# Kernel optimization log

Hardware: AMD Instinct MI355X
Metric: run time of the kernel (lower is better)

The kernel has to match this reference:

```python
import jax, jax.numpy as jnp
import numpy as np

B, T, NF, D, H = 4, 32, 256, 512, 8
DK = D // H


def setup_inputs() -> dict:
    key = jax.random.key(0)
    ks = jax.random.split(key, 10)
    x = jax.random.normal(ks[0], (B, T, NF, D), dtype=jnp.float32)
    adj = jax.random.randint(ks[1], (NF, NF), 0, 2, dtype=jnp.int32)
    adj = adj.at[jnp.arange(NF), jnp.arange(NF)].set(1)  # self-loops avoid all-masked rows
    s = 1.0 / np.sqrt(D)
    Wq = jax.random.normal(ks[2], (D, D), dtype=jnp.float32) * s
    Wk = jax.random.normal(ks[3], (D, D), dtype=jnp.float32) * s
    Wv = jax.random.normal(ks[4], (D, D), dtype=jnp.float32) * s
    Wo = jax.random.normal(ks[5], (D, D), dtype=jnp.float32) * s
    bq = jnp.zeros((D,), jnp.float32)
    bk = jnp.zeros((D,), jnp.float32)
    bv = jnp.zeros((D,), jnp.float32)
    bo = jnp.zeros((D,), jnp.float32)
    return {"x": x, "adj": adj, "Wq": Wq, "bq": bq, "Wk": Wk, "bk": bk,
            "Wv": Wv, "bv": bv, "Wo": Wo, "bo": bo}


def reference(x, adj, Wq, bq, Wk, bk, Wv, bv, Wo, bo):
    b, t, nf, d = x.shape
    q = x @ Wq.T + bq
    k = x @ Wk.T + bk
    v = x @ Wv.T + bv
    # split heads: [B,T,Nf,H,dk]
    qh = q.reshape(b, t, nf, H, DK)
    kh = k.reshape(b, t, nf, H, DK)
    vh = v.reshape(b, t, nf, H, DK)
    scores = jnp.einsum('btihd,btjhd->bthij', qh, kh) / jnp.sqrt(jnp.float32(DK))
    mask = (adj > 0)  # [Nf,Nf], broadcast over b,t,h
    scores = jnp.where(mask[None, None, None], scores, jnp.float32(-jnp.inf))
    attn = jax.nn.softmax(scores, axis=-1)  # dropout is identity in eval
    out = jnp.einsum('bthij,btjhd->btihd', attn, vh).reshape(b, t, nf, d)
    return out @ Wo.T + bo
```

## Files before the change

### kernel.cpp

```cpp
#include <hip/hip_runtime.h>

#define NF 256
#define H_ 8
#define M_ 32768

typedef _Float16 f16;
typedef _Float16 f16x8 __attribute__((ext_vector_type(8)));
typedef float f32x4 __attribute__((ext_vector_type(4)));
typedef unsigned short u16x8 __attribute__((ext_vector_type(8)));

#define GLOAD16(src, dst) \
  __builtin_amdgcn_global_load_lds((const __attribute__((address_space(1))) void*)(src), \
                                   (__attribute__((address_space(3))) void*)(dst), 16, 0, 0)

#define LDS_FENCE() do { asm volatile("s_waitcnt lgkmcnt(0)" ::: "memory"); \
                         __builtin_amdgcn_sched_barrier(0); } while (0)

template <int NR>
__device__ __forceinline__ void stage_rows(const f16* __restrict__ g, int ld, int row0, int coff,
                                           f16* ldsb, int wave, int lane) {
    const int rr = wave * 8 + (lane >> 3);
    const int p  = lane & 7;
#pragma unroll
    for (int i = 0; i < NR / 32; ++i) {
        int r = i * 32 + rr;
        int col = ((p ^ (r & 7)) << 3);
        GLOAD16(g + (size_t)(row0 + r) * ld + coff + col, ldsb + (i * 32 + wave * 8) * 64);
    }
}

template <int NR>
__device__ __forceinline__ void stage_rows512(const f16* __restrict__ g, int ld, int coff,
                                              f16* ldsb, int wave, int lane) {
    const int rr = wave * 8 + (lane >> 3);
    const int p  = lane & 7;
#pragma unroll
    for (int i = 0; i < NR / 64; ++i) {
        int r = i * 64 + rr;
        int col = ((p ^ (r & 7)) << 3);
        GLOAD16(g + (size_t)r * ld + coff + col, ldsb + (i * 64 + wave * 8) * 64);
    }
}


__global__ void cvt_x(const float* __restrict__ src, f16* __restrict__ dst, int n8) {
    int idx = blockIdx.x * blockDim.x + threadIdx.x;
    int stride = gridDim.x * blockDim.x;
    for (; idx < n8; idx += stride) {
        const float4* s = reinterpret_cast<const float4*>(src + (size_t)idx * 8);
        float4 v0 = s[0], v1 = s[1];
        f16x8 o;
        o[0] = (f16)v0.x; o[1] = (f16)v0.y; o[2] = (f16)v0.z; o[3] = (f16)v0.w;
        o[4] = (f16)v1.x; o[5] = (f16)v1.y; o[6] = (f16)v1.z; o[7] = (f16)v1.w;
        *reinterpret_cast<f16x8*>(dst + (size_t)idx * 8) = o;
    }
}

#define QSCALE 0.1803368801111204f

__global__ void prep(const float* __restrict__ Wq, const float* __restrict__ Wk,
                     const float* __restrict__ Wv, const float* __restrict__ Wo,
                     const float* __restrict__ bq, const float* __restrict__ bk,
                     const float* __restrict__ bv, const int* __restrict__ adj,
                     f16* __restrict__ Wh, f16* __restrict__ Woh,
                     float* __restrict__ biasAll, unsigned long long* __restrict__ bmask) {
    const int tid = blockIdx.x * 256 + threadIdx.x;
    {
        const float* s; f16* d; float sc = 1.0f;
        int pp = tid >> 15, off = tid & 32767;
        if (pp == 0)      { s = Wq; d = Wh;              sc = QSCALE; }
        else if (pp == 1) { s = Wk; d = Wh + 512 * 512; }
        else if (pp == 2) { s = Wv; d = Wh + 2 * 512 * 512; }
        else              { s = Wo; d = Woh; }
        const float4* sv4 = reinterpret_cast<const float4*>(s + (size_t)off * 8);
        float4 v0 = sv4[0], v1 = sv4[1];
        f16x8 o;
        o[0] = (f16)(v0.x * sc); o[1] = (f16)(v0.y * sc);
        o[2] = (f16)(v0.z * sc); o[3] = (f16)(v0.w * sc);
        o[4] = (f16)(v1.x * sc); o[5] = (f16)(v1.y * sc);
        o[6] = (f16)(v1.z * sc); o[7] = (f16)(v1.w * sc);
        *reinterpret_cast<f16x8*>(d + (size_t)off * 8) = o;
    }
    if (tid < 1536) {
        float v = (tid < 512) ? QSCALE * bq[tid] : (tid < 1024) ? bk[tid - 512] : bv[tid - 1024];
        biasAll[tid] = v;
    }
    if (tid < 65536) {
        unsigned long long bal = __ballot(adj[tid] > 0);
        if ((tid & 63) == 0) bmask[tid >> 6] = bal;
    }
}


__global__ __launch_bounds__(256) void qkv_gemm(const f16* __restrict__ A, const f16* __restrict__ W,
                                                const float* __restrict__ biasAll,
                                                f16* __restrict__ out) {
    __shared__ f16 lds[32768];
    const int t = threadIdx.x, wave = t >> 6, lane = t & 63;
    const int l15 = lane & 15, l4 = lane >> 4;
    const int m0 = blockIdx.x * 128, n0 = blockIdx.y * 128;
    const int wr = wave >> 1, wc = wave & 1;
    f32x4 acc[4][4] = {};

    stage_rows<128>(A, 512, m0, 0, lds, wave, lane);
    stage_rows<128>(W, 512, n0, 0, lds + 8192, wave, lane);
    __syncthreads();
    int cur = 0;
    for (int kt = 0; kt < 8; ++kt) {
        if (kt < 7) {
            stage_rows<128>(A, 512, m0, (kt + 1) * 64, lds + (cur ^ 1) * 16384, wave, lane);
            stage_rows<128>(W, 512, n0, (kt + 1) * 64, lds + (cur ^ 1) * 16384 + 8192, wave, lane);
        }
        const f16* Ab = lds + cur * 16384;
        const f16* Bb = Ab + 8192;
        f16x8 af[4][2], bf[4][2];
#pragma unroll
        for (int i = 0; i < 4; ++i)
#pragma unroll
            for (int kk = 0; kk < 2; ++kk) {
                int ra = wr * 64 + i * 16 + l15;
                int rb = wc * 64 + i * 16 + l15;
                int s = kk * 4 + l4;
                af[i][kk] = *reinterpret_cast<const f16x8*>(Ab + ra * 64 + ((s ^ (ra & 7)) << 3));
                bf[i][kk] = *reinterpret_cast<const f16x8*>(Bb + rb * 64 + ((s ^ (rb & 7)) << 3));
            }
#pragma unroll
        for (int i = 0; i < 4; ++i)
#pragma unroll
            for (int j = 0; j < 4; ++j)
#pragma unroll
                for (int kk = 0; kk < 2; ++kk)
                    acc[i][j] = __builtin_amdgcn_mfma_f32_16x16x32_f16(af[i][kk], bf[j][kk], acc[i][j], 0, 0, 0);
        __syncthreads();
        cur ^= 1;
    }
    {
        f16* Es = lds;
#pragma unroll
        for (int i = 0; i < 4; ++i)
#pragma unroll
            for (int j = 0; j < 4; ++j) {
                int lc = wc * 64 + j * 16 + l15;
                float bb = biasAll[n0 + lc];
#pragma unroll
                for (int r = 0; r < 4; ++r) {
                    int lr = wr * 64 + i * 16 + l4 * 4 + r;
                    Es[lr * 132 + lc] = (f16)(acc[i][j][r] + bb);
                }
            }
        __syncthreads();
        const int rrow = t >> 4, slot = t & 15;
#pragma unroll
        for (int p2 = 0; p2 < 8; ++p2) {
            int r = p2 * 16 + rrow;
            *reinterpret_cast<f16x8*>(out + (size_t)(m0 + r) * 1536 + n0 + slot * 8) =
                *reinterpret_cast<const f16x8*>(Es + r * 132 + slot * 8);
        }
    }
}


__global__ __launch_bounds__(512) void attn_kernel(const f16* __restrict__ qkv,
                                                   const unsigned long long* __restrict__ bmg,
                                                   f16* __restrict__ ao) {
    __shared__ f16 Ks[256 * 64];
    __shared__ f16 Vs[64 * 256];
    __shared__ f16 Ps[8][16][264];
    __shared__ unsigned long long BMs[1024];
    const int t = threadIdx.x, wave = t >> 6, lane = t & 63;
    const int l15 = lane & 15, l4 = lane >> 4;
    const int bh = blockIdx.x, bt = bh >> 3, h = bh & 7;
    const int btq = bt * 256, hq = h * 64;
    const f16* qb = qkv + (size_t)btq * 1536 + hq;
    const f16* kb = qkv + (size_t)btq * 1536 + 512 + hq;
    const f16* vb = qkv + (size_t)btq * 1536 + 1024 + hq;

    stage_rows512<256>(kb, 1536, 0, Ks, wave, lane);
    GLOAD16((const char*)bmg + (size_t)t * 16, (char*)(BMs + wave * 128));
    {
        const int slot = t & 7, r0 = t >> 3;
#pragma unroll
        for (int i = 0; i < 4; ++i) {
            int nf = r0 + i * 64;
            f16x8 v = *reinterpret_cast<const f16x8*>(vb + (size_t)nf * 1536 + slot * 8);
#pragma unroll
            for (int e = 0; e < 8; ++e) {
                int dk = slot * 8 + e;
                int key = (dk & 7) ^ (dk >> 3);
                Vs[dk * 256 + (((nf >> 3) ^ key) << 3) + (nf & 7)] = v[e];
            }
        }
    }
    __syncthreads();

    for (int s = 0; s < 2; ++s) {
        const int qrow_base = wave * 32 + s * 16;

        f16x8 aq[2];
#pragma unroll
        for (int kk = 0; kk < 2; ++kk)
            aq[kk] = *reinterpret_cast<const f16x8*>(
                qb + (size_t)(qrow_base + l15) * 1536 + kk * 32 + l4 * 8);

        f32x4 sacc[16];
#pragma unroll
        for (int ct = 0; ct < 16; ++ct) sacc[ct] = (f32x4){0.f, 0.f, 0.f, 0.f};
#pragma unroll
        for (int ct = 0; ct < 16; ++ct)
#pragma unroll
            for (int kk = 0; kk < 2; ++kk) {
                int rk = ct * 16 + l15;
                int sk = kk * 4 + l4;
                f16x8 bk_ = *reinterpret_cast<const f16x8*>(Ks + rk * 64 + ((sk ^ (rk & 7)) << 3));
                sacc[ct] = __builtin_amdgcn_mfma_f32_16x16x32_f16(aq[kk], bk_, sacc[ct], 0, 0, 0);
            }

        LDS_FENCE();

        float rs[4];
#pragma unroll
        for (int r = 0; r < 4; ++r) {
            const int ig = qrow_base + l4 * 4 + r;
            const u16x8* mr = reinterpret_cast<const u16x8*>(BMs + ig * 4);
            u16x8 w0 = mr[0], w1 = mr[1];
            float mx = -1e38f;
#pragma unroll
            for (int ct = 0; ct < 16; ++ct) mx = fmaxf(mx, sacc[ct][r]);
#pragma unroll
            for (int m = 1; m < 16; m <<= 1) mx = fmaxf(mx, __shfl_xor(mx, m, 64));
            float sum = 0.f;
#pragma unroll
            for (int ct = 0; ct < 16; ++ct) {
                unsigned wbit = (ct < 8) ? (unsigned)w0[ct] : (unsigned)w1[ct & 7];
                float p = __builtin_exp2f(sacc[ct][r] - mx);
                p = ((wbit >> l15) & 1u) ? p : 0.0f;
                sacc[ct][r] = p;
                sum += p;
            }
#pragma unroll
            for (int m = 1; m < 16; m <<= 1) sum += __shfl_xor(sum, m, 64);
            rs[r] = 1.0f / sum;
#pragma unroll
            for (int ct = 0; ct < 16; ++ct)
                Ps[wave][l4 * 4 + r][ct * 16 + l15] = (f16)sacc[ct][r];
        }

        LDS_FENCE();

        f32x4 oacc[4] = {};
#pragma unroll
        for (int kk = 0; kk < 8; ++kk) {
            f16x8 ap = *reinterpret_cast<const f16x8*>(&Ps[wave][l15][kk * 32 + l4 * 8]);
#pragma unroll
            for (int c2 = 0; c2 < 4; ++c2) {
                int dk = c2 * 16 + l15;
                int key = (dk & 7) ^ (dk >> 3);
                int sv = kk * 4 + l4;
                f16x8 bv_ = *reinterpret_cast<const f16x8*>(Vs + dk * 256 + ((sv ^ key) << 3));
                oacc[c2] = __builtin_amdgcn_mfma_f32_16x16x32_f16(ap, bv_, oacc[c2], 0, 0, 0);
            }
        }
#pragma unroll
        for (int c2 = 0; c2 < 4; ++c2)
#pragma unroll
            for (int r = 0; r < 4; ++r) {
                int nf = qrow_base + l4 * 4 + r;
                int dcol = hq + c2 * 16 + l15;
                ao[((size_t)btq + nf) * 512 + dcol] = (f16)(oacc[c2][r] * rs[r]);
            }
    }
}


__global__ __launch_bounds__(256) void o_gemm(const f16* __restrict__ A, const f16* __restrict__ W,
                                              const float* __restrict__ bo, float* __restrict__ out) {
    __shared__ f16 lds[32768];
    const int t = threadIdx.x, wave = t >> 6, lane = t & 63;
    const int l15 = lane & 15, l4 = lane >> 4;
    const int m0 = blockIdx.x * 128, n0 = blockIdx.y * 128;
    const int wr = wave >> 1, wc = wave & 1;
    f32x4 acc[4][4] = {};

    stage_rows<128>(A, 512, m0, 0, lds, wave, lane);
    stage_rows<128>(W, 512, n0, 0, lds + 8192, wave, lane);
    __syncthreads();
    int cur = 0;
    for (int kt = 0; kt < 8; ++kt) {
        if (kt < 7) {
            stage_rows<128>(A, 512, m0, (kt + 1) * 64, lds + (cur ^ 1) * 16384, wave, lane);
            stage_rows<128>(W, 512, n0, (kt + 1) * 64, lds + (cur ^ 1) * 16384 + 8192, wave, lane);
        }
        const f16* Ab = lds + cur * 16384;
        const f16* Bb = Ab + 8192;
        f16x8 af[4][2], bf[4][2];
#pragma unroll
        for (int i = 0; i < 4; ++i)
#pragma unroll
            for (int kk = 0; kk < 2; ++kk) {
                int ra = wr * 64 + i * 16 + l15;
                int rb = wc * 64 + i * 16 + l15;
                int s = kk * 4 + l4;
                af[i][kk] = *reinterpret_cast<const f16x8*>(Ab + ra * 64 + ((s ^ (ra & 7)) << 3));
                bf[i][kk] = *reinterpret_cast<const f16x8*>(Bb + rb * 64 + ((s ^ (rb & 7)) << 3));
            }
#pragma unroll
        for (int i = 0; i < 4; ++i)
#pragma unroll
            for (int j = 0; j < 4; ++j)
#pragma unroll
                for (int kk = 0; kk < 2; ++kk)
                    acc[i][j] = __builtin_amdgcn_mfma_f32_16x16x32_f16(af[i][kk], bf[j][kk], acc[i][j], 0, 0, 0);
        __syncthreads();
        cur ^= 1;
    }
#pragma unroll
    for (int i = 0; i < 4; ++i)
#pragma unroll
        for (int j = 0; j < 4; ++j) {
            int ng = n0 + wc * 64 + j * 16 + l15;
            float bb = bo[ng];
#pragma unroll
            for (int r = 0; r < 4; ++r) {
                int mg = m0 + wr * 64 + i * 16 + l4 * 4 + r;
                out[(size_t)mg * 512 + ng] = acc[i][j][r] + bb;
            }
        }
}


extern "C" void kernel_launch(void* const* d_in, const int* in_sizes, int n_in,
                              void* d_out, int out_size, void* d_ws, size_t ws_size,
                              hipStream_t stream) {
    const float* x   = (const float*)d_in[0];
    const int*   adj = (const int*)d_in[1];
    const float* Wq  = (const float*)d_in[2];
    const float* bq  = (const float*)d_in[3];
    const float* Wk  = (const float*)d_in[4];
    const float* bk  = (const float*)d_in[5];
    const float* Wv  = (const float*)d_in[6];
    const float* bv  = (const float*)d_in[7];
    const float* Wo  = (const float*)d_in[8];
    const float* bo  = (const float*)d_in[9];
    float* out = (float*)d_out;

    char* ws = (char*)d_ws;
    f16*   Wh      = (f16*)ws;
    f16*   Woh     = (f16*)(ws + 1572864);
    float* biasAll = (float*)(ws + 2097152);
    unsigned long long* bmask = (unsigned long long*)(ws + 2103296);
    f16*   xh      = (f16*)(ws + 2111488);
    f16*   qkvb    = (f16*)(ws + 2111488 + (size_t)M_ * 512 * 2);
    f16*   aob     = xh;

    cvt_x<<<2048, 256, 0, stream>>>(x, xh, M_ * 512 / 8);
    prep<<<512, 256, 0, stream>>>(Wq, Wk, Wv, Wo, bq, bk, bv, adj, Wh, Woh, biasAll, bmask);
    qkv_gemm<<<dim3(M_ / 128, 12), 256, 0, stream>>>(xh, Wh, biasAll, qkvb);
    attn_kernel<<<128 * H_, 512, 0, stream>>>(qkvb, bmask, aob);
    o_gemm<<<dim3(M_ / 128, 4), 256, 0, stream>>>(aob, Woh, bo, out);
}
```

Measured before the change: 204.1 us.

## Halve GEMM K-tile to shrink LDS and remap blocks for XCD locality

Both GEMMs move from a K-tile of 64 to 32, which halves the double-buffered LDS footprint (64KB to 32KB, with a union for the qkv epilogue) and uses a new 4-chunk swizzle. This is meant to let more blocks be resident per CU. The grid becomes 1D with an XCD-aware mapping so blocks sharing A rows land on the same XCD and reuse L2. The cost is twice as many K iterations and barriers, with fewer MFMAs between each sync.

```diff
diff --git a/kernel.cpp b/kernel.cpp
--- a/kernel.cpp
+++ b/kernel.cpp
@@ -17,15 +17,15 @@
                          __builtin_amdgcn_sched_barrier(0); } while (0)
 
 template <int NR>
-__device__ __forceinline__ void stage_rows(const f16* __restrict__ g, int ld, int row0, int coff,
-                                           f16* ldsb, int wave, int lane) {
-    const int rr = wave * 8 + (lane >> 3);
-    const int p  = lane & 7;
-#pragma unroll
-    for (int i = 0; i < NR / 32; ++i) {
-        int r = i * 32 + rr;
-        int col = ((p ^ (r & 7)) << 3);
-        GLOAD16(g + (size_t)(row0 + r) * ld + coff + col, ldsb + (i * 32 + wave * 8) * 64);
+__device__ __forceinline__ void stage32(const f16* __restrict__ g, int ld, int row0, int coff,
+                                        f16* ldsb, int wave, int lane) {
+    const int rr = wave * 16 + (lane >> 2);
+    const int p  = lane & 3;
+#pragma unroll
+    for (int i = 0; i < NR / 64; ++i) {
+        int r = i * 64 + rr;
+        int col = ((p ^ ((r >> 1) & 3)) << 3);
+        GLOAD16(g + (size_t)(row0 + r) * ld + coff + col, ldsb + (i * 64 + wave * 16) * 32);
     }
 }
 
@@ -95,47 +95,48 @@
 __global__ __launch_bounds__(256) void qkv_gemm(const f16* __restrict__ A, const f16* __restrict__ W,
                                                 const float* __restrict__ biasAll,
                                                 f16* __restrict__ out) {
-    __shared__ f16 lds[32768];
+    __shared__ union { f16 stage[16384]; f16 epi[128 * 132]; } u;
     const int t = threadIdx.x, wave = t >> 6, lane = t & 63;
     const int l15 = lane & 15, l4 = lane >> 4;
-    const int m0 = blockIdx.x * 128, n0 = blockIdx.y * 128;
+    const int lb = blockIdx.x;
+    const int xcd = lb & 7, idx = lb >> 3;
+    const int m0 = (xcd * 32 + idx / 12) * 128;
+    const int n0 = (idx % 12) * 128;
     const int wr = wave >> 1, wc = wave & 1;
     f32x4 acc[4][4] = {};
 
-    stage_rows<128>(A, 512, m0, 0, lds, wave, lane);
-    stage_rows<128>(W, 512, n0, 0, lds + 8192, wave, lane);
+    stage32<128>(A, 512, m0, 0, u.stage, wave, lane);
+    stage32<128>(W, 512, n0, 0, u.stage + 4096, wave, lane);
     __syncthreads();
     int cur = 0;
-    for (int kt = 0; kt < 8; ++kt) {
-        if (kt < 7) {
-            stage_rows<128>(A, 512, m0, (kt + 1) * 64, lds + (cur ^ 1) * 16384, wave, lane);
-            stage_rows<128>(W, 512, n0, (kt + 1) * 64, lds + (cur ^ 1) * 16384 + 8192, wave, lane);
-        }
-        const f16* Ab = lds + cur * 16384;
-        const f16* Bb = Ab + 8192;
-        f16x8 af[4][2], bf[4][2];
+    for (int kt = 0; kt < 16; ++kt) {
+        if (kt < 15) {
+            stage32<128>(A, 512, m0, (kt + 1) * 32, u.stage + (cur ^ 1) * 8192, wave, lane);
+            stage32<128>(W, 512, n0, (kt + 1) * 32, u.stage + (cur ^ 1) * 8192 + 4096, wave, lane);
+        }
+        const f16* Ab = u.stage + cur * 8192;
+        const f16* Bb = Ab + 4096;
+        f16x8 af[4], bf[4];
+#pragma unroll
+        for (int i = 0; i < 4; ++i) {
+            int ra = wr * 64 + i * 16 + l15;
+            af[i] = *reinterpret_cast<const f16x8*>(Ab + ra * 32 + ((l4 ^ ((ra >> 1) & 3)) << 3));
+        }
+#pragma unroll
+        for (int j = 0; j < 4; ++j) {
+            int rb = wc * 64 + j * 16 + l15;
+            bf[j] = *reinterpret_cast<const f16x8*>(Bb + rb * 32 + ((l4 ^ ((rb >> 1) & 3)) << 3));
+        }
 #pragma unroll
         for (int i = 0; i < 4; ++i)
 #pragma unroll
-            for (int kk = 0; kk < 2; ++kk) {
-                int ra = wr * 64 + i * 16 + l15;
-                int rb = wc * 64 + i * 16 + l15;
-                int s = kk * 4 + l4;
-                af[i][kk] = *reinterpret_cast<const f16x8*>(Ab + ra * 64 + ((s ^ (ra & 7)) << 3));
-                bf[i][kk] = *reinterpret_cast<const f16x8*>(Bb + rb * 64 + ((s ^ (rb & 7)) << 3));
-            }
-#pragma unroll
-        for (int i = 0; i < 4; ++i)
-#pragma unroll
             for (int j = 0; j < 4; ++j)
-#pragma unroll
-                for (int kk = 0; kk < 2; ++kk)
-                    acc[i][j] = __builtin_amdgcn_mfma_f32_16x16x32_f16(af[i][kk], bf[j][kk], acc[i][j], 0, 0, 0);
+                acc[i][j] = __builtin_amdgcn_mfma_f32_16x16x32_f16(af[i], bf[j], acc[i][j], 0, 0, 0);
         __syncthreads();
         cur ^= 1;
     }
     {
-        f16* Es = lds;
+        f16* Es = u.epi;
 #pragma unroll
         for (int i = 0; i < 4; ++i)
 #pragma unroll
@@ -274,42 +275,43 @@
 
 __global__ __launch_bounds__(256) void o_gemm(const f16* __restrict__ A, const f16* __restrict__ W,
                                               const float* __restrict__ bo, float* __restrict__ out) {
-    __shared__ f16 lds[32768];
+    __shared__ f16 lds[16384];
     const int t = threadIdx.x, wave = t >> 6, lane = t & 63;
     const int l15 = lane & 15, l4 = lane >> 4;
-    const int m0 = blockIdx.x * 128, n0 = blockIdx.y * 128;
+    const int lb = blockIdx.x;
+    const int xcd = lb & 7, idx = lb >> 3;
+    const int m0 = (xcd * 32 + idx / 4) * 128;
+    const int n0 = (idx % 4) * 128;
     const int wr = wave >> 1, wc = wave & 1;
     f32x4 acc[4][4] = {};
 
-    stage_rows<128>(A, 512, m0, 0, lds, wave, lane);
-    stage_rows<128>(W, 512, n0, 0, lds + 8192, wave, lane);
+    stage32<128>(A, 512, m0, 0, lds, wave, lane);
+    stage32<128>(W, 512, n0, 0, lds + 4096, wave, lane);
     __syncthreads();
     int cur = 0;
-    for (int kt = 0; kt < 8; ++kt) {
-        if (kt < 7) {
-            stage_rows<128>(A, 512, m0, (kt + 1) * 64, lds + (cur ^ 1) * 16384, wave, lane);
-            stage_rows<128>(W, 512, n0, (kt + 1) * 64, lds + (cur ^ 1) * 16384 + 8192, wave, lane);
-        }
-        const f16* Ab = lds + cur * 16384;
-        const f16* Bb = Ab + 8192;
-        f16x8 af[4][2], bf[4][2];
+    for (int kt = 0; kt < 16; ++kt) {
+        if (kt < 15) {
+            stage32<128>(A, 512, m0, (kt + 1) * 32, lds + (cur ^ 1) * 8192, wave, lane);
+            stage32<128>(W, 512, n0, (kt + 1) * 32, lds + (cur ^ 1) * 8192 + 4096, wave, lane);
+        }
+        const f16* Ab = lds + cur * 8192;
+        const f16* Bb = Ab + 4096;
+        f16x8 af[4], bf[4];
+#pragma unroll
+        for (int i = 0; i < 4; ++i) {
+            int ra = wr * 64 + i * 16 + l15;
+            af[i] = *reinterpret_cast<const f16x8*>(Ab + ra * 32 + ((l4 ^ ((ra >> 1) & 3)) << 3));
+        }
+#pragma unroll
+        for (int j = 0; j < 4; ++j) {
+            int rb = wc * 64 + j * 16 + l15;
+            bf[j] = *reinterpret_cast<const f16x8*>(Bb + rb * 32 + ((l4 ^ ((rb >> 1) & 3)) << 3));
+        }
 #pragma unroll
         for (int i = 0; i < 4; ++i)
 #pragma unroll
-            for (int kk = 0; kk < 2; ++kk) {
-                int ra = wr * 64 + i * 16 + l15;
-                int rb = wc * 64 + i * 16 + l15;
-                int s = kk * 4 + l4;
-                af[i][kk] = *reinterpret_cast<const f16x8*>(Ab + ra * 64 + ((s ^ (ra & 7)) << 3));
-                bf[i][kk] = *reinterpret_cast<const f16x8*>(Bb + rb * 64 + ((s ^ (rb & 7)) << 3));
-            }
-#pragma unroll
-        for (int i = 0; i < 4; ++i)
-#pragma unroll
             for (int j = 0; j < 4; ++j)
-#pragma unroll
-                for (int kk = 0; kk < 2; ++kk)
-                    acc[i][j] = __builtin_amdgcn_mfma_f32_16x16x32_f16(af[i][kk], bf[j][kk], acc[i][j], 0, 0, 0);
+                acc[i][j] = __builtin_amdgcn_mfma_f32_16x16x32_f16(af[i], bf[j], acc[i][j], 0, 0, 0);
         __syncthreads();
         cur ^= 1;
     }
@@ -354,7 +356,7 @@
 
     cvt_x<<<2048, 256, 0, stream>>>(x, xh, M_ * 512 / 8);
     prep<<<512, 256, 0, stream>>>(Wq, Wk, Wv, Wo, bq, bk, bv, adj, Wh, Woh, biasAll, bmask);
-    qkv_gemm<<<dim3(M_ / 128, 12), 256, 0, stream>>>(xh, Wh, biasAll, qkvb);
+    qkv_gemm<<<3072, 256, 0, stream>>>(xh, Wh, biasAll, qkvb);
     attn_kernel<<<128 * H_, 512, 0, stream>>>(qkvb, bmask, aob);
-    o_gemm<<<dim3(M_ / 128, 4), 256, 0, stream>>>(aob, Woh, bo, out);
-}
+    o_gemm<<<1024, 256, 0, stream>>>(aob, Woh, bo, out);
+}
```

Measured after the change: 190.8 us. -6.5%, faster.

## Use 256x256 tiled GEMM core with staggered prefetch and XCD-aware block mapping

Applied to the files above, without the earlier changes.

The QKV and output-projection GEMMs move from 128x128 tiles with 4 waves to 256x256 tiles with 8 waves, sharing one core routine. That routine prefetches A and W chunks at staggered points inside the MFMA loop, uses raw barriers with partial vmcnt waits, and raises wave priority around the MFMA bursts. Block indices are remapped so that neighbouring M tiles land on the same XCD, and the x conversion is merged into the weight-prep kernel to save a launch. Larger tiles cut global and L2 traffic per FLOP, but they double LDS use to 128KB and raise register pressure, which lowers occupancy and leaves fewer blocks in the grid.

```diff
diff --git a/kernel.cpp b/kernel.cpp
--- a/kernel.cpp
+++ b/kernel.cpp
@@ -15,56 +15,105 @@
 
 #define LDS_FENCE() do { asm volatile("s_waitcnt lgkmcnt(0)" ::: "memory"); \
                          __builtin_amdgcn_sched_barrier(0); } while (0)
-
-template <int NR>
-__device__ __forceinline__ void stage_rows(const f16* __restrict__ g, int ld, int row0, int coff,
-                                           f16* ldsb, int wave, int lane) {
-    const int rr = wave * 8 + (lane >> 3);
-    const int p  = lane & 7;
-#pragma unroll
-    for (int i = 0; i < NR / 32; ++i) {
-        int r = i * 32 + rr;
-        int col = ((p ^ (r & 7)) << 3);
-        GLOAD16(g + (size_t)(row0 + r) * ld + coff + col, ldsb + (i * 32 + wave * 8) * 64);
-    }
-}
-
-template <int NR>
-__device__ __forceinline__ void stage_rows512(const f16* __restrict__ g, int ld, int coff,
-                                              f16* ldsb, int wave, int lane) {
-    const int rr = wave * 8 + (lane >> 3);
-    const int p  = lane & 7;
-#pragma unroll
-    for (int i = 0; i < NR / 64; ++i) {
-        int r = i * 64 + rr;
-        int col = ((p ^ (r & 7)) << 3);
-        GLOAD16(g + (size_t)r * ld + coff + col, ldsb + (i * 64 + wave * 8) * 64);
-    }
-}
-
-
-__global__ void cvt_x(const float* __restrict__ src, f16* __restrict__ dst, int n8) {
-    int idx = blockIdx.x * blockDim.x + threadIdx.x;
-    int stride = gridDim.x * blockDim.x;
-    for (; idx < n8; idx += stride) {
-        const float4* s = reinterpret_cast<const float4*>(src + (size_t)idx * 8);
-        float4 v0 = s[0], v1 = s[1];
-        f16x8 o;
-        o[0] = (f16)v0.x; o[1] = (f16)v0.y; o[2] = (f16)v0.z; o[3] = (f16)v0.w;
-        o[4] = (f16)v1.x; o[5] = (f16)v1.y; o[6] = (f16)v1.z; o[7] = (f16)v1.w;
-        *reinterpret_cast<f16x8*>(dst + (size_t)idx * 8) = o;
-    }
-}
+#define SBAR() asm volatile("s_barrier" ::: "memory")
+
+
+__device__ __forceinline__ void stageHT(const f16* __restrict__ g, int r0, int k0,
+                                        f16* ldst, int wave, int lane) {
+    const int key = lane >> 3;
+    const int colsw = k0 + (((lane & 7) ^ key) << 3);
+#pragma unroll
+    for (int i = 0; i < 2; ++i) {
+        int r = i * 64 + wave * 8 + key;
+        GLOAD16(g + (size_t)(r0 + r) * 512 + colsw, ldst + (i * 64 + wave * 8) * 64);
+    }
+}
+
+__device__ __forceinline__ void gemm256_core(const f16* __restrict__ A, const f16* __restrict__ W,
+                                             int m0, int n0, f16* lds,
+                                             f32x4 (&acc)[8][4], int wave, int lane) {
+    const int wr = wave & 1, wc = wave >> 1;
+    const int l15 = lane & 15, l4 = lane >> 4;
+    stageHT(W, n0,        0, lds + 16384, wave, lane);
+    stageHT(W, n0 + 128,  0, lds + 24576, wave, lane);
+    stageHT(A, m0,        0, lds,         wave, lane);
+    stageHT(A, m0 + 128,  0, lds + 8192,  wave, lane);
+    stageHT(W, n0,       64, lds + 32768 + 16384, wave, lane);
+    stageHT(W, n0 + 128, 64, lds + 32768 + 24576, wave, lane);
+    asm volatile("s_waitcnt vmcnt(4)" ::: "memory");
+    SBAR();
+#pragma unroll
+    for (int t = 0; t < 8; ++t) {
+        f16* bufA = lds + (t & 1) * 32768;
+        f16* bufB = bufA + 16384;
+        f16* nA   = lds + ((t & 1) ^ 1) * 32768;
+        f16x8 bfr[4][2];
+#pragma unroll
+        for (int j = 0; j < 4; ++j)
+#pragma unroll
+            for (int kk = 0; kk < 2; ++kk) {
+                int rb = wc * 64 + j * 16 + l15;
+                bfr[j][kk] = *reinterpret_cast<const f16x8*>(
+                    bufB + rb * 64 + ((((kk << 2) + l4) ^ (rb & 7)) << 3));
+            }
+#pragma unroll
+        for (int q = 0; q < 4; ++q) {
+            f16x8 afr[2][2];
+#pragma unroll
+            for (int rf = 0; rf < 2; ++rf)
+#pragma unroll
+                for (int kk = 0; kk < 2; ++kk) {
+                    int ra = wr * 128 + q * 32 + rf * 16 + l15;
+                    afr[rf][kk] = *reinterpret_cast<const f16x8*>(
+                        bufA + ra * 64 + ((((kk << 2) + l4) ^ (ra & 7)) << 3));
+                }
+            if (q == 0 && t < 7) stageHT(A, m0,       (t + 1) * 64, nA,          wave, lane);
+            if (q == 1 && t < 7) stageHT(A, m0 + 128, (t + 1) * 64, nA + 8192,   wave, lane);
+            if (q == 2 && t < 6) stageHT(W, n0,       (t + 2) * 64, bufB,        wave, lane);
+            if (q == 3 && t < 6) stageHT(W, n0 + 128, (t + 2) * 64, bufB + 8192, wave, lane);
+            SBAR();
+            LDS_FENCE();
+            __builtin_amdgcn_s_setprio(1);
+#pragma unroll
+            for (int rf = 0; rf < 2; ++rf)
+#pragma unroll
+                for (int j = 0; j < 4; ++j)
+#pragma unroll
+                    for (int kk = 0; kk < 2; ++kk)
+                        acc[q * 2 + rf][j] = __builtin_amdgcn_mfma_f32_16x16x32_f16(
+                            afr[rf][kk], bfr[j][kk], acc[q * 2 + rf][j], 0, 0, 0);
+            __builtin_amdgcn_s_setprio(0);
+            if (q < 3) SBAR();
+        }
+        if (t < 6) { asm volatile("s_waitcnt vmcnt(4)" ::: "memory"); }
+        else       { asm volatile("s_waitcnt vmcnt(0)" ::: "memory"); }
+        SBAR();
+    }
+}
+
 
 #define QSCALE 0.1803368801111204f
 
-__global__ void prep(const float* __restrict__ Wq, const float* __restrict__ Wk,
-                     const float* __restrict__ Wv, const float* __restrict__ Wo,
-                     const float* __restrict__ bq, const float* __restrict__ bk,
-                     const float* __restrict__ bv, const int* __restrict__ adj,
-                     f16* __restrict__ Wh, f16* __restrict__ Woh,
-                     float* __restrict__ biasAll, unsigned long long* __restrict__ bmask) {
-    const int tid = blockIdx.x * 256 + threadIdx.x;
+__global__ void prep_all(const float* __restrict__ x, f16* __restrict__ xh,
+                         const float* __restrict__ Wq, const float* __restrict__ Wk,
+                         const float* __restrict__ Wv, const float* __restrict__ Wo,
+                         const float* __restrict__ bq, const float* __restrict__ bk,
+                         const float* __restrict__ bv, const int* __restrict__ adj,
+                         f16* __restrict__ Wh, f16* __restrict__ Woh,
+                         float* __restrict__ biasAll, unsigned long long* __restrict__ bmask) {
+    if (blockIdx.x < 2048) {
+        int idx = blockIdx.x * 256 + threadIdx.x;
+        for (; idx < M_ * 512 / 8; idx += 2048 * 256) {
+            const float4* s = reinterpret_cast<const float4*>(x + (size_t)idx * 8);
+            float4 v0 = s[0], v1 = s[1];
+            f16x8 o;
+            o[0] = (f16)v0.x; o[1] = (f16)v0.y; o[2] = (f16)v0.z; o[3] = (f16)v0.w;
+            o[4] = (f16)v1.x; o[5] = (f16)v1.y; o[6] = (f16)v1.z; o[7] = (f16)v1.w;
+            *reinterpret_cast<f16x8*>(xh + (size_t)idx * 8) = o;
+        }
+        return;
+    }
+    const int tid = (blockIdx.x - 2048) * 256 + threadIdx.x;
     {
         const float* s; f16* d; float sc = 1.0f;
         int pp = tid >> 15, off = tid & 32767;
@@ -92,73 +141,61 @@
 }
 
 
-__global__ __launch_bounds__(256) void qkv_gemm(const f16* __restrict__ A, const f16* __restrict__ W,
+__global__ __launch_bounds__(512) void qkv_gemm(const f16* __restrict__ A, const f16* __restrict__ W,
                                                 const float* __restrict__ biasAll,
                                                 f16* __restrict__ out) {
-    __shared__ f16 lds[32768];
-    const int t = threadIdx.x, wave = t >> 6, lane = t & 63;
+    __shared__ __align__(16) f16 lds[65536];
+    const int tt = threadIdx.x, wave = tt >> 6, lane = tt & 63;
+    const int lb = blockIdx.x, xcd = lb & 7, idx = lb >> 3;
+    const int m0 = (xcd * 16 + idx / 6) * 256;
+    const int n0 = (idx % 6) * 256;
+    f32x4 acc[8][4] = {};
+    gemm256_core(A, W, m0, n0, lds, acc, wave, lane);
+
+    const int wr = wave & 1, wc = wave >> 1;
     const int l15 = lane & 15, l4 = lane >> 4;
-    const int m0 = blockIdx.x * 128, n0 = blockIdx.y * 128;
-    const int wr = wave >> 1, wc = wave & 1;
-    f32x4 acc[4][4] = {};
-
-    stage_rows<128>(A, 512, m0, 0, lds, wave, lane);
-    stage_rows<128>(W, 512, n0, 0, lds + 8192, wave, lane);
-    __syncthreads();
-    int cur = 0;
-    for (int kt = 0; kt < 8; ++kt) {
-        if (kt < 7) {
-            stage_rows<128>(A, 512, m0, (kt + 1) * 64, lds + (cur ^ 1) * 16384, wave, lane);
-            stage_rows<128>(W, 512, n0, (kt + 1) * 64, lds + (cur ^ 1) * 16384 + 8192, wave, lane);
-        }
-        const f16* Ab = lds + cur * 16384;
-        const f16* Bb = Ab + 8192;
-        f16x8 af[4][2], bf[4][2];
-#pragma unroll
-        for (int i = 0; i < 4; ++i)
-#pragma unroll
-            for (int kk = 0; kk < 2; ++kk) {
-                int ra = wr * 64 + i * 16 + l15;
-                int rb = wc * 64 + i * 16 + l15;
-                int s = kk * 4 + l4;
-                af[i][kk] = *reinterpret_cast<const f16x8*>(Ab + ra * 64 + ((s ^ (ra & 7)) << 3));
-                bf[i][kk] = *reinterpret_cast<const f16x8*>(Bb + rb * 64 + ((s ^ (rb & 7)) << 3));
-            }
-#pragma unroll
-        for (int i = 0; i < 4; ++i)
-#pragma unroll
-            for (int j = 0; j < 4; ++j)
-#pragma unroll
-                for (int kk = 0; kk < 2; ++kk)
-                    acc[i][j] = __builtin_amdgcn_mfma_f32_16x16x32_f16(af[i][kk], bf[j][kk], acc[i][j], 0, 0, 0);
-        __syncthreads();
-        cur ^= 1;
-    }
-    {
-        f16* Es = lds;
-#pragma unroll
-        for (int i = 0; i < 4; ++i)
-#pragma unroll
-            for (int j = 0; j < 4; ++j) {
-                int lc = wc * 64 + j * 16 + l15;
-                float bb = biasAll[n0 + lc];
-#pragma unroll
-                for (int r = 0; r < 4; ++r) {
-                    int lr = wr * 64 + i * 16 + l4 * 4 + r;
-                    Es[lr * 132 + lc] = (f16)(acc[i][j][r] + bb);
-                }
-            }
-        __syncthreads();
-        const int rrow = t >> 4, slot = t & 15;
-#pragma unroll
-        for (int p2 = 0; p2 < 8; ++p2) {
-            int r = p2 * 16 + rrow;
-            *reinterpret_cast<f16x8*>(out + (size_t)(m0 + r) * 1536 + n0 + slot * 8) =
-                *reinterpret_cast<const f16x8*>(Es + r * 132 + slot * 8);
-        }
-    }
-}
-
+    f16* epi = lds;
+    float bb[4];
+#pragma unroll
+    for (int bc = 0; bc < 4; ++bc) bb[bc] = biasAll[n0 + wc * 64 + bc * 16 + l15];
+#pragma unroll
+    for (int half = 0; half < 2; ++half) {
+        if (wr == half) {
+#pragma unroll
+            for (int ar = 0; ar < 8; ++ar)
+#pragma unroll
+                for (int bc = 0; bc < 4; ++bc)
+#pragma unroll
+                    for (int r = 0; r < 4; ++r)
+                        epi[(ar * 16 + l4 * 4 + r) * 264 + wc * 64 + bc * 16 + l15] =
+                            (f16)(acc[ar][bc][r] + bb[bc]);
+        }
+        LDS_FENCE();
+        SBAR();
+        const int rr = tt >> 5, slot = tt & 31;
+#pragma unroll
+        for (int p = 0; p < 8; ++p) {
+            int row = p * 16 + rr;
+            *reinterpret_cast<f16x8*>(out + (size_t)(m0 + half * 128 + row) * 1536 + n0 + slot * 8) =
+                *reinterpret_cast<const f16x8*>(epi + row * 264 + slot * 8);
+        }
+        SBAR();
+    }
+}
+
+
+template <int NR>
+__device__ __forceinline__ void stage_rows512(const f16* __restrict__ g, int ld, int coff,
+                                              f16* ldsb, int wave, int lane) {
+    const int rr = wave * 8 + (lane >> 3);
+    const int p  = lane & 7;
+#pragma unroll
+    for (int i = 0; i < NR / 64; ++i) {
+        int r = i * 64 + rr;
+        int col = ((p ^ (r & 7)) << 3);
+        GLOAD16(g + (size_t)r * ld + coff + col, ldsb + (i * 64 + wave * 8) * 64);
+    }
+}
 
 __global__ __launch_bounds__(512) void attn_kernel(const f16* __restrict__ qkv,
                                                    const unsigned long long* __restrict__ bmg,
@@ -272,57 +309,30 @@
 }
 
 
-__global__ __launch_bounds__(256) void o_gemm(const f16* __restrict__ A, const f16* __restrict__ W,
+__global__ __launch_bounds__(512) void o_gemm(const f16* __restrict__ A, const f16* __restrict__ W,
                                               const float* __restrict__ bo, float* __restrict__ out) {
-    __shared__ f16 lds[32768];
-    const int t = threadIdx.x, wave = t >> 6, lane = t & 63;
+    __shared__ __align__(16) f16 lds[65536];
+    const int tt = threadIdx.x, wave = tt >> 6, lane = tt & 63;
+    const int lb = blockIdx.x, xcd = lb & 7, idx = lb >> 3;
+    const int m0 = (xcd * 16 + idx / 2) * 256;
+    const int n0 = (idx % 2) * 256;
+    f32x4 acc[8][4] = {};
+    gemm256_core(A, W, m0, n0, lds, acc, wave, lane);
+
+    const int wr = wave & 1, wc = wave >> 1;
     const int l15 = lane & 15, l4 = lane >> 4;
-    const int m0 = blockIdx.x * 128, n0 = blockIdx.y * 128;
-    const int wr = wave >> 1, wc = wave & 1;
-    f32x4 acc[4][4] = {};
-
-    stage_rows<128>(A, 512, m0, 0, lds, wave, lane);
-    stage_rows<128>(W, 512, n0, 0, lds + 8192, wave, lane);
-    __syncthreads();
-    int cur = 0;
-    for (int kt = 0; kt < 8; ++kt) {
-        if (kt < 7) {
-            stage_rows<128>(A, 512, m0, (kt + 1) * 64, lds + (cur ^ 1) * 16384, wave, lane);
-            stage_rows<128>(W, 512, n0, (kt + 1) * 64, lds + (cur ^ 1) * 16384 + 8192, wave, lane);
-        }
-        const f16* Ab = lds + cur * 16384;
-        const f16* Bb = Ab + 8192;
-        f16x8 af[4][2], bf[4][2];
-#pragma unroll
-        for (int i = 0; i < 4; ++i)
-#pragma unroll
-            for (int kk = 0; kk < 2; ++kk) {
-                int ra = wr * 64 + i * 16 + l15;
-                int rb = wc * 64 + i * 16 + l15;
-                int s = kk * 4 + l4;
-                af[i][kk] = *reinterpret_cast<const f16x8*>(Ab + ra * 64 + ((s ^ (ra & 7)) << 3));
-                bf[i][kk] = *reinterpret_cast<const f16x8*>(Bb + rb * 64 + ((s ^ (rb & 7)) << 3));
-            }
-#pragma unroll
-        for (int i = 0; i < 4; ++i)
-#pragma unroll
-            for (int j = 0; j < 4; ++j)
-#pragma unroll
-                for (int kk = 0; kk < 2; ++kk)
-                    acc[i][j] = __builtin_amdgcn_mfma_f32_16x16x32_f16(af[i][kk], bf[j][kk], acc[i][j], 0, 0, 0);
-        __syncthreads();
-        cur ^= 1;
-    }
-#pragma unroll
-    for (int i = 0; i < 4; ++i)
-#pragma unroll
-        for (int j = 0; j < 4; ++j) {
-            int ng = n0 + wc * 64 + j * 16 + l15;
-            float bb = bo[ng];
+    float bb[4];
+#pragma unroll
+    for (int bc = 0; bc < 4; ++bc) bb[bc] = bo[n0 + wc * 64 + bc * 16 + l15];
+#pragma unroll
+    for (int ar = 0; ar < 8; ++ar)
+#pragma unroll
+        for (int bc = 0; bc < 4; ++bc) {
+            int ng = n0 + wc * 64 + bc * 16 + l15;
 #pragma unroll
             for (int r = 0; r < 4; ++r) {
-                int mg = m0 + wr * 64 + i * 16 + l4 * 4 + r;
-                out[(size_t)mg * 512 + ng] = acc[i][j][r] + bb;
+                int mg = m0 + wr * 128 + ar * 16 + l4 * 4 + r;
+                out[(size_t)mg * 512 + ng] = acc[ar][bc][r] + bb[bc];
             }
         }
 }
@@ -352,9 +362,9 @@
     f16*   qkvb    = (f16*)(ws + 2111488 + (size_t)M_ * 512 * 2);
     f16*   aob     = xh;
 
-    cvt_x<<<2048, 256, 0, stream>>>(x, xh, M_ * 512 / 8);
-    prep<<<512, 256, 0, stream>>>(Wq, Wk, Wv, Wo, bq, bk, bv, adj, Wh, Woh, biasAll, bmask);
-    qkv_gemm<<<dim3(M_ / 128, 12), 256, 0, stream>>>(xh, Wh, biasAll, qkvb);
+    prep_all<<<2560, 256, 0, stream>>>(x, xh, Wq, Wk, Wv, Wo, bq, bk, bv, adj,
+                                       Wh, Woh, biasAll, bmask);
+    qkv_gemm<<<768, 512, 0, stream>>>(xh, Wh, biasAll, qkvb);
     attn_kernel<<<128 * H_, 512, 0, stream>>>(qkvb, bmask, aob);
-    o_gemm<<<dim3(M_ / 128, 4), 256, 0, stream>>>(aob, Woh, bo, out);
-}
+    o_gemm<<<256, 512, 0, stream>>>(aob, Woh, bo, out);
+}
```

After: 182.3 us. 1.12x faster.
